# Performance work log

Measured on AMD Instinct MI355X. Metric: run time of the kernel, lower is better.

Reference implementation:

```python
import jax, jax.numpy as jnp
import numpy as np

EPS = 1e-6
NUM_HEADS = 16


def layer_norm(x, a, b):
    # Faithful to the custom LayerNorm: unbiased std (ddof=1), eps added to sigma.
    mu = jnp.mean(x, axis=-1, keepdims=True)
    sigma = jnp.std(x, axis=-1, keepdims=True, ddof=1) + EPS
    return (x - mu) / sigma * a + b


def entmax15(x):
    # Exact 1.5-entmax along the last axis (Peters et al. 2019, sort-based).
    S = x.shape[-1]
    x = x / 2.0
    x = x - jnp.max(x, axis=-1, keepdims=True)  # shift-invariant stabilization
    xs = jnp.flip(jnp.sort(x, axis=-1), axis=-1)  # descending
    k = jnp.arange(1, S + 1, dtype=x.dtype)
    mean = jnp.cumsum(xs, axis=-1) / k
    meansq = jnp.cumsum(xs * xs, axis=-1) / k
    ss = k * (meansq - mean * mean)
    delta = (1.0 - ss) / k
    tau = mean - jnp.sqrt(jnp.clip(delta, 0.0))
    support_size = jnp.sum((tau <= xs).astype(jnp.int32), axis=-1, keepdims=True)
    tau_star = jnp.take_along_axis(tau, support_size - 1, axis=-1)
    return jnp.clip(x - tau_star, 0.0) ** 2


def linear(x, w, b):
    return jnp.einsum('bsd,od->bso', x, w) + b


def setup_inputs() -> dict:
    key = jax.random.key(0)
    B, S, D, DFF = 1, 2048, 1024, 4096
    ks = jax.random.split(key, 12)
    p = lambda k, shape: jax.random.normal(k, shape, dtype=jnp.float32) * 0.02
    return {
        'inputs': jax.random.normal(ks[0], (B, S, D), dtype=jnp.float32),
        'mask': jax.random.randint(ks[1], (B, S), 0, 2, dtype=jnp.int32),
        'wq': p(ks[2], (D, D)), 'bq': jnp.zeros((D,), jnp.float32),
        'wk': p(ks[3], (D, D)), 'bk': jnp.zeros((D,), jnp.float32),
        'wv': p(ks[4], (D, D)), 'bv': jnp.zeros((D,), jnp.float32),
        'wo': p(ks[5], (D, D)), 'bo': jnp.zeros((D,), jnp.float32),
        'ln1_a': jnp.ones((D,), jnp.float32), 'ln1_b': jnp.zeros((D,), jnp.float32),
        'w1': p(ks[6], (DFF, D)), 'b1': jnp.zeros((DFF,), jnp.float32),
        'w2': p(ks[7], (D, DFF)), 'b2': jnp.zeros((D,), jnp.float32),
        'ln2_a': jnp.ones((D,), jnp.float32), 'ln2_b': jnp.zeros((D,), jnp.float32),
    }


def reference(inputs, mask, wq, bq, wk, bk, wv, bv, wo, bo, ln1_a, ln1_b,
              w1, b1, w2, b2, ln2_a, ln2_b):
    B, S, D = inputs.shape
    H = NUM_HEADS
    hd = D // H

    # --- Sublayer 1: pre-norm -> SparseMHA -> residual (dropout=0 -> identity) ---
    x1 = layer_norm(inputs, ln1_a, ln1_b)
    split = lambda t: t.reshape(B, S, H, hd).transpose(0, 2, 1, 3)  # [B,H,S,hd]
    q = split(linear(x1, wq, bq))
    k = split(linear(x1, wk, bk))
    v = split(linear(x1, wv, bv))

    scores = jnp.einsum('bhqd,bhkd->bhqk', q, k) / jnp.sqrt(jnp.asarray(hd, jnp.float32))
    # torch: mask.unsqueeze(0) -> (1,B,S); with B==1 it broadcasts as a key mask (1,1,1,S)
    mask4 = mask[None, None]  # (1,1,B,S), B==1
    scores = jnp.where(mask4 == 0, jnp.float32(-1e9), scores)

    p_attn = entmax15(scores).astype(jnp.float32)
    attended = jnp.einsum('bhqk,bhkd->bhqd', p_attn, v)
    attended = attended.transpose(0, 2, 1, 3).reshape(B, S, D)
    y = inputs + linear(attended, wo, bo)

    # --- Sublayer 2: pre-norm -> FFN -> residual ---
    x2 = layer_norm(y, ln2_a, ln2_b)
    ffn = linear(jax.nn.relu(linear(x2, w1, b1)), w2, b2)
    return y + ffn
```

## Files before the change

### kernel.cpp

```cpp
#include <hip/hip_runtime.h>
#include <hip/hip_bf16.h>

#define S   2048
#define D   1024
#define DFF 4096
#define NH  16
#define HD  64

typedef unsigned short u16;
typedef unsigned int   u32;
typedef __attribute__((ext_vector_type(8))) short      short8;
typedef __attribute__((ext_vector_type(4))) float      floatx4;
typedef __attribute__((ext_vector_type(2))) _Float16   half2v;
typedef __attribute__((ext_vector_type(4))) _Float16   half4v;
typedef __attribute__((ext_vector_type(8))) _Float16   half8v;

__device__ __forceinline__ float bu2f(u16 u) {
    union { u32 i; float f; } x; x.i = ((u32)u) << 16; return x.f;
}
__device__ __forceinline__ u16 f2bu(float f) {
    __hip_bfloat16 h = __float2bfloat16(f);
    return *(u16*)&h;
}
__device__ __forceinline__ u16 f2h(float f) {
    _Float16 h = (_Float16)f; return *(u16*)&h;
}
__device__ __forceinline__ float ldf(const float* p) { return *p; }
__device__ __forceinline__ float ldf(const u16* p)   { return bu2f(*p); }

__device__ __forceinline__ half2v pkrtz(float a, float b) {
    auto v = __builtin_amdgcn_cvt_pkrtz(a, b);
    union { decltype(v) i; half2v o; } u; u.i = v; return u.o;
}

__device__ __forceinline__ floatx4 mfma_f16(half8v a, half8v b, floatx4 c) {
    return __builtin_amdgcn_mfma_f32_16x16x32_f16(a, b, c, 0, 0, 0);
}
__device__ __forceinline__ float fdot2f(half2v a, half2v b, float c) {
#if __has_builtin(__builtin_amdgcn_fdot2)
    return __builtin_amdgcn_fdot2(a, b, c, false);
#else
    return c + (float)a[0] * (float)b[0] + (float)a[1] * (float)b[1];
#endif
}

template <int K>
__device__ __forceinline__ float ror16f(float v) {
    int s = __builtin_bit_cast(int, v);
    int r = __builtin_amdgcn_update_dpp(s, s, 0x120 | K, 0xF, 0xF, false);
    return __builtin_bit_cast(float, r);
}
__device__ __forceinline__ float rowsum16(float v) {
    v += ror16f<1>(v);
    v += ror16f<2>(v);
    v += ror16f<4>(v);
    v += ror16f<8>(v);
    return v;
}
__device__ __forceinline__ float rowmax16(float v) {
    v = fmaxf(v, ror16f<1>(v));
    v = fmaxf(v, ror16f<2>(v));
    v = fmaxf(v, ror16f<4>(v));
    v = fmaxf(v, ror16f<8>(v));
    return v;
}

__device__ __forceinline__ void async16(const void* g, void* l) {
    __builtin_amdgcn_global_load_lds(
        (const __attribute__((address_space(1))) u32*)g,
        (__attribute__((address_space(3))) u32*)l, 16, 0, 0);
}

#define WAITV(N) asm volatile("s_waitcnt vmcnt(" N ")" ::: "memory")
#define WAITL()  asm volatile("s_waitcnt lgkmcnt(0)" ::: "memory")
#define SBAR()   __builtin_amdgcn_s_barrier()
#define SCHED0() __builtin_amdgcn_sched_barrier(0)

__global__ __launch_bounds__(256)
void cvt_kernel(const float* __restrict__ in, u16* __restrict__ out, int n4)
{
    int i = blockIdx.x * 256 + threadIdx.x;
    if (i < n4) {
        float4 v = ((const float4*)in)[i];
        ushort4 s;
        s.x = f2bu(v.x); s.y = f2bu(v.y); s.z = f2bu(v.z); s.w = f2bu(v.w);
        ((ushort4*)out)[i] = s;
    }
}

__global__ __launch_bounds__(256)
void prep_kernel(const int* __restrict__ mask, int* __restrict__ newpos,
                 int* __restrict__ nkbuf,
                 const float* __restrict__ wq, const float* __restrict__ wk,
                 const float* __restrict__ wv, const float* __restrict__ wo,
                 u16* __restrict__ wqkvb, u16* __restrict__ wob)
{
    const int blk = blockIdx.x;
    const int t = threadIdx.x;
    if (blk == 0) {
        __shared__ int ps[256];
        int loc[8];
        int s = 0;
#pragma unroll
        for (int j = 0; j < 8; j++) {
            loc[j] = s;
            s += (mask[t * 8 + j] != 0);
        }
        ps[t] = s;
        __syncthreads();
        for (int off = 1; off < 256; off <<= 1) {
            int v = (t >= off) ? ps[t - off] : 0;
            __syncthreads();
            ps[t] += v;
            __syncthreads();
        }
        const int total = ps[255];
        const int base = t ? ps[t - 1] : 0;
#pragma unroll
        for (int j = 0; j < 8; j++) {
            const int gi = t * 8 + j;
            const int up = base + loc[j];
            newpos[gi] = mask[gi] ? up : (total + gi - up);
        }
        if (t == 0) nkbuf[0] = total;
    } else {
        int cb = blk - 1;
        const float* src;
        u16* dst;
        if (cb < 1024)      { src = wq; dst = wqkvb; }
        else if (cb < 2048) { src = wk; dst = wqkvb + 1024 * 1024; cb -= 1024; }
        else if (cb < 3072) { src = wv; dst = wqkvb + 2 * 1024 * 1024; cb -= 2048; }
        else                { src = wo; dst = wob; cb -= 3072; }
        const int i = cb * 256 + t;
        float4 v = ((const float4*)src)[i];
        ushort4 sv;
        sv.x = f2bu(v.x); sv.y = f2bu(v.y); sv.z = f2bu(v.z); sv.w = f2bu(v.w);
        ((ushort4*)dst)[i] = sv;
    }
}

template <typename T>
__global__ __launch_bounds__(256, 4)
void ln_kernel(const T* __restrict__ in, const float* __restrict__ ga,
               const float* __restrict__ gb, u16* __restrict__ out)
{
    const int row = blockIdx.x;
    const int t = threadIdx.x;
    const T* x = in + (size_t)row * D;
    float v[4];
    float s = 0.f, ss = 0.f;
#pragma unroll
    for (int j = 0; j < 4; j++) {
        float val = ldf(x + t + 256 * j);
        v[j] = val; s += val; ss = fmaf(val, val, ss);
    }
#pragma unroll
    for (int off = 32; off >= 1; off >>= 1) {
        s  += __shfl_down(s,  off, 64);
        ss += __shfl_down(ss, off, 64);
    }
    __shared__ float red[10];
    const int wave = t >> 6, lane = t & 63;
    if (lane == 0) { red[wave] = s; red[4 + wave] = ss; }
    __syncthreads();
    if (t == 0) {
        float S1 = red[0] + red[1] + red[2] + red[3];
        float S2 = red[4] + red[5] + red[6] + red[7];
        float mu = S1 / (float)D;
        float var = (S2 - (float)D * mu * mu) / (float)(D - 1);
        float sig = sqrtf(fmaxf(var, 0.f)) + 1e-6f;
        red[8] = mu; red[9] = 1.f / sig;
    }
    __syncthreads();
    const float mu = red[8], rs = red[9];
#pragma unroll
    for (int j = 0; j < 4; j++) {
        int c = t + 256 * j;
        out[(size_t)row * D + c] = f2bu((v[j] - mu) * rs * ga[c] + gb[c]);
    }
}

#define GEMM_CORE(A_, B_, K_)                                                   \
    __shared__ u16 As[3 * 128 * 32];                                            \
    __shared__ u16 Bs[3 * 128 * 32];                                            \
    const int t = threadIdx.x;                                                  \
    const int w = t >> 6, l = t & 63;                                           \
    const int m0 = blockIdx.y * 128, n0 = blockIdx.x * 128;                     \
    const int qk = l >> 4, col = l & 15;                                        \
    const int wm = (w & 1) * 64, wn = (w >> 1) * 64;                            \
    const int sr  = l >> 2;                                                     \
    const int sq  = l & 3;                                                      \
    const int row = w * 16 + sr;                                                \
    const int gq  = sq ^ ((row >> 1) & 3);                                      \
    const u16* Ap = A_ + (size_t)(m0 + row) * K_ + gq * 8;                      \
    const u16* Bp = B_ + (size_t)(n0 + row) * K_ + gq * 8;                      \
    u16* AsW = As + w * 16 * 32;                                                \
    u16* BsW = Bs + w * 16 * 32;                                                \
    const int mloc = wm + col, nloc = wn + col;                                 \
    const int aoff = mloc * 32 + (qk ^ ((mloc >> 1) & 3)) * 8;                  \
    const int boff = nloc * 32 + (qk ^ ((nloc >> 1) & 3)) * 8;                  \
    floatx4 acc[4][4];                                                          \
    _Pragma("unroll")                                                           \
    for (int i = 0; i < 4; i++)                                                 \
        _Pragma("unroll")                                                       \
        for (int j = 0; j < 4; j++) acc[i][j] = (floatx4)0.f;                   \
    const int NT_ = K_ / 32;                                                    \
    _Pragma("unroll")                                                           \
    for (int s = 0; s < 3; s++) {                                               \
        async16(Ap,                   AsW + s * 4096);                          \
        async16(Ap + (size_t)64 * K_, AsW + s * 4096 + 64 * 32);                \
        async16(Bp,                   BsW + s * 4096);                          \
        async16(Bp + (size_t)64 * K_, BsW + s * 4096 + 64 * 32);                \
        Ap += 32; Bp += 32;                                                     \
    }                                                                           \
    WAITV("8"); SCHED0(); SBAR();                                               \
    int cur = 0;                                                                \
    for (int t0 = 0; t0 + 3 < NT_; ++t0) {                                      \
        short8 a[4], b[4];                                                      \
        const u16* aB = As + cur * 4096 + aoff;                                 \
        const u16* bB = Bs + cur * 4096 + boff;                                 \
        _Pragma("unroll")                                                       \
        for (int i = 0; i < 4; i++) a[i] = *(const short8*)(aB + i * 16 * 32);  \
        _Pragma("unroll")                                                       \
        for (int j = 0; j < 4; j++) b[j] = *(const short8*)(bB + j * 16 * 32);  \
        WAITL(); SCHED0(); SBAR();                                              \
        async16(Ap,                   AsW + cur * 4096);                        \
        async16(Ap + (size_t)64 * K_, AsW + cur * 4096 + 64 * 32);              \
        async16(Bp,                   BsW + cur * 4096);                        \
        async16(Bp + (size_t)64 * K_, BsW + cur * 4096 + 64 * 32);              \
        Ap += 32; Bp += 32;                                                     \
        _Pragma("unroll")                                                       \
        for (int i = 0; i < 4; i++)                                             \
            _Pragma("unroll")                                                   \
            for (int j = 0; j < 4; j++)                                         \
                acc[i][j] = __builtin_amdgcn_mfma_f32_16x16x32_bf16(            \
                    a[i], b[j], acc[i][j], 0, 0, 0);                            \
        WAITV("8"); SCHED0(); SBAR();                                           \
        cur = cur + 1; if (cur == 3) cur = 0;                                   \
    }                                                                           \
    _Pragma("unroll")                                                           \
    for (int tail = 0; tail < 3; tail++) {                                      \
        short8 a[4], b[4];                                                      \
        const u16* aB = As + cur * 4096 + aoff;                                 \
        const u16* bB = Bs + cur * 4096 + boff;                                 \
        _Pragma("unroll")                                                       \
        for (int i = 0; i < 4; i++) a[i] = *(const short8*)(aB + i * 16 * 32);  \
        _Pragma("unroll")                                                       \
        for (int j = 0; j < 4; j++) b[j] = *(const short8*)(bB + j * 16 * 32);  \
        _Pragma("unroll")                                                       \
        for (int i = 0; i < 4; i++)                                             \
            _Pragma("unroll")                                                   \
            for (int j = 0; j < 4; j++)                                         \
                acc[i][j] = __builtin_amdgcn_mfma_f32_16x16x32_bf16(            \
                    a[i], b[j], acc[i][j], 0, 0, 0);                            \
        if (tail == 0) { WAITV("4"); SCHED0(); SBAR(); }                        \
        if (tail == 1) { WAITV("0"); SCHED0(); SBAR(); }                        \
        cur = cur + 1; if (cur == 3) cur = 0;                                   \
    }

template <int OMODE, bool RELU, int RES>
__global__ __launch_bounds__(256, 2)
void gemm_mfma(const u16* __restrict__ A, const u16* __restrict__ B,
               const float* __restrict__ bias, const void* __restrict__ res,
               void* __restrict__ Cout, int M, int N, int K)
{
    GEMM_CORE(A, B, K)
#pragma unroll
    for (int j = 0; j < 4; j++) {
        const int n = n0 + wn + j * 16 + col;
        const float bn = bias[n];
#pragma unroll
        for (int i = 0; i < 4; i++) {
#pragma unroll
            for (int r = 0; r < 4; r++) {
                const int m = m0 + wm + i * 16 + qk * 4 + r;
                float v = acc[i][j][r] + bn;
                if (RELU) v = fmaxf(v, 0.f);
                if (RES == 1) v += ((const float*)res)[(size_t)m * N + n];
                if (RES == 2) v += bu2f(((const u16*)res)[(size_t)m * N + n]);
                if (OMODE == 0) ((float*)Cout)[(size_t)m * N + n] = v;
                if (OMODE == 1) ((u16*)Cout)[(size_t)m * N + n] = f2bu(v);
            }
        }
    }
}

__global__ __launch_bounds__(256, 2)
void gemm_qkv(const u16* __restrict__ A, const u16* __restrict__ B,
              const float* __restrict__ bq, const float* __restrict__ bk,
              const float* __restrict__ bv, const int* __restrict__ np,
              u16* __restrict__ outQ, u16* __restrict__ outK,
              u16* __restrict__ outVT)
{
    const int K = D;
    GEMM_CORE(A, B, K)
    const int seg   = n0 >> 10;
    const int nbase = n0 & 1023;
    const float* bs = (seg == 0) ? bq : (seg == 1) ? bk : bv;
    int npm[4][4];
    if (seg != 0) {
#pragma unroll
        for (int i = 0; i < 4; i++)
#pragma unroll
            for (int r = 0; r < 4; r++)
                npm[i][r] = np[m0 + wm + i * 16 + qk * 4 + r];
    }
#pragma unroll
    for (int j = 0; j < 4; j++) {
        const int nl = nbase + wn + j * 16 + col;
        const float bn = bs[nl];
#pragma unroll
        for (int i = 0; i < 4; i++) {
#pragma unroll
            for (int r = 0; r < 4; r++) {
                const int m = m0 + wm + i * 16 + qk * 4 + r;
                float v = acc[i][j][r] + bn;
                if (seg == 0)      outQ [(size_t)m * D + nl]          = f2h(v);
                else if (seg == 1) outK [(size_t)npm[i][r] * D + nl]  = f2h(v);
                else               outVT[(size_t)nl * S + npm[i][r]]  = f2h(v);
            }
        }
    }
}

template <int OMODE, int RES>
__global__ __launch_bounds__(256, 2)
void gemm_mfma64(const u16* __restrict__ A, const u16* __restrict__ B,
                 const float* __restrict__ bias, const void* __restrict__ res,
                 void* __restrict__ Cout, int M, int N, int K)
{
    __shared__ u16 As[3 * 128 * 32];
    __shared__ u16 Bs[3 * 64 * 32];
    const int t = threadIdx.x;
    const int w = t >> 6, l = t & 63;
    const int m0 = blockIdx.y * 128, n0 = blockIdx.x * 64;
    const int qk = l >> 4, col = l & 15;
    const int wm = (w & 1) * 64, wn = (w >> 1) * 32;
    const int sr = l >> 2, sq = l & 3;
    const int row = w * 16 + sr;
    const int gq = sq ^ ((row >> 1) & 3);
    const u16* Ap = A + (size_t)(m0 + row) * K + gq * 8;
    const u16* Bp = B + (size_t)(n0 + row) * K + gq * 8;
    u16* AsW = As + w * 16 * 32;
    u16* BsW = Bs + w * 16 * 32;
    const int mloc = wm + col, nloc = wn + col;
    const int aoff = mloc * 32 + (qk ^ ((mloc >> 1) & 3)) * 8;
    const int boff = nloc * 32 + (qk ^ ((nloc >> 1) & 3)) * 8;
    floatx4 acc[4][2];
#pragma unroll
    for (int i = 0; i < 4; i++)
#pragma unroll
        for (int j = 0; j < 2; j++) acc[i][j] = (floatx4)0.f;
    const int NT_ = K / 32;
#pragma unroll
    for (int s = 0; s < 3; s++) {
        async16(Ap,                  AsW + s * 4096);
        async16(Ap + (size_t)64 * K, AsW + s * 4096 + 64 * 32);
        async16(Bp,                  BsW + s * 2048);
        Ap += 32; Bp += 32;
    }
    WAITV("6"); SCHED0(); SBAR();
    int cur = 0;
    for (int t0 = 0; t0 + 3 < NT_; ++t0) {
        short8 a[4], b[2];
        const u16* aB = As + cur * 4096 + aoff;
        const u16* bB = Bs + cur * 2048 + boff;
#pragma unroll
        for (int i = 0; i < 4; i++) a[i] = *(const short8*)(aB + i * 16 * 32);
#pragma unroll
        for (int j = 0; j < 2; j++) b[j] = *(const short8*)(bB + j * 16 * 32);
        WAITL(); SCHED0(); SBAR();
        async16(Ap,                  AsW + cur * 4096);
        async16(Ap + (size_t)64 * K, AsW + cur * 4096 + 64 * 32);
        async16(Bp,                  BsW + cur * 2048);
        Ap += 32; Bp += 32;
#pragma unroll
        for (int i = 0; i < 4; i++)
#pragma unroll
            for (int j = 0; j < 2; j++)
                acc[i][j] = __builtin_amdgcn_mfma_f32_16x16x32_bf16(
                    a[i], b[j], acc[i][j], 0, 0, 0);
        WAITV("6"); SCHED0(); SBAR();
        cur = cur + 1; if (cur == 3) cur = 0;
    }
#pragma unroll
    for (int tail = 0; tail < 3; tail++) {
        short8 a[4], b[2];
        const u16* aB = As + cur * 4096 + aoff;
        const u16* bB = Bs + cur * 2048 + boff;
#pragma unroll
        for (int i = 0; i < 4; i++) a[i] = *(const short8*)(aB + i * 16 * 32);
#pragma unroll
        for (int j = 0; j < 2; j++) b[j] = *(const short8*)(bB + j * 16 * 32);
#pragma unroll
        for (int i = 0; i < 4; i++)
#pragma unroll
            for (int j = 0; j < 2; j++)
                acc[i][j] = __builtin_amdgcn_mfma_f32_16x16x32_bf16(
                    a[i], b[j], acc[i][j], 0, 0, 0);
        if (tail == 0) { WAITV("3"); SCHED0(); SBAR(); }
        if (tail == 1) { WAITV("0"); SCHED0(); SBAR(); }
        cur = cur + 1; if (cur == 3) cur = 0;
    }
#pragma unroll
    for (int j = 0; j < 2; j++) {
        const int n = n0 + wn + j * 16 + col;
        const float bn = bias[n];
#pragma unroll
        for (int i = 0; i < 4; i++) {
#pragma unroll
            for (int r = 0; r < 4; r++) {
                const int m = m0 + wm + i * 16 + qk * 4 + r;
                float v = acc[i][j][r] + bn;
                if (RES == 1) v += ((const float*)res)[(size_t)m * N + n];
                if (RES == 2) v += bu2f(((const u16*)res)[(size_t)m * N + n]);
                if (OMODE == 0) ((float*)Cout)[(size_t)m * N + n] = v;
                if (OMODE == 1) ((u16*)Cout)[(size_t)m * N + n] = f2bu(v);
            }
        }
    }
}

__global__ __launch_bounds__(256, 3)
void attn_cvt(const u16* __restrict__ qb, const u16* __restrict__ kb,
              const u16* __restrict__ vT, const int* __restrict__ nkbuf,
              u16* __restrict__ att,
              const float* __restrict__ w1src, u16* __restrict__ w1dst)
{
    __shared__ u16 Plds[16 * 1024];
    const int blk = blockIdx.x;
    const int t  = threadIdx.x;
    if (blk >= 2048) {
        const int i = (blk - 2048) * 256 + t;
        float4 v = ((const float4*)w1src)[i];
        ushort4 sv;
        sv.x = f2bu(v.x); sv.y = f2bu(v.y); sv.z = f2bu(v.z); sv.w = f2bu(v.w);
        ((ushort4*)w1dst)[i] = sv;
        return;
    }
    const int nk = nkbuf[0];
    const int NS = (nk + 127) >> 7;
    const int NT = (nk + 31) >> 5;
    const int hh = blk >> 7;
    const int q0 = (blk & 127) * 16;
    const int w  = __builtin_amdgcn_readfirstlane(t >> 6);
    const int l  = t & 63;
    const int lg = l >> 4, lc = l & 15;
    const _Float16 NEG = (_Float16)(-30000.f);
    const half4v NEG4 = {NEG, NEG, NEG, NEG};

    const u16* qp = qb + (size_t)(q0 + lc) * D + hh * HD + lg * 8;
    const half8v bq0 = *(const half8v*)qp;
    const half8v bq1 = *(const half8v*)(qp + 32);
    const u16* kbase = kb + hh * HD + lg * 8;
    const int R = 4 * w + lg;
    const half2v one2 = {(_Float16)1.f, (_Float16)1.f};
    const u16* vp = vT + (size_t)(hh * HD + w * 16 + lc) * S + lg * 8;

    if (nk <= 1152) {
#pragma unroll
        for (int T = 0; T < 16; T++) {
            const int g = 4 * T + w;
            if (g < 8 * NS) {
                half4v scv;
                if ((g + 1) * 16 <= nk) {
                    const u16* kp = kbase + (size_t)(g * 16 + lc) * D;
                    floatx4 a = (floatx4)0.f;
                    a = mfma_f16(*(const half8v*)kp,        bq0, a);
                    a = mfma_f16(*(const half8v*)(kp + 32), bq1, a);
                    half2v p01 = pkrtz(a[0] * 0.0625f, a[1] * 0.0625f);
                    half2v p23 = pkrtz(a[2] * 0.0625f, a[3] * 0.0625f);
                    scv = __builtin_shufflevector(p01, p23, 0, 1, 2, 3);
                } else if (g * 16 < nk) {
                    const u16* kp = kbase + (size_t)(g * 16 + lc) * D;
                    floatx4 a = (floatx4)0.f;
                    a = mfma_f16(*(const half8v*)kp,        bq0, a);
                    a = mfma_f16(*(const half8v*)(kp + 32), bq1, a);
                    const int kb0 = g * 16 + lg * 4;
                    half2v p01 = pkrtz(kb0 + 0 < nk ? a[0] * 0.0625f : -30000.f,
                                       kb0 + 1 < nk ? a[1] * 0.0625f : -30000.f);
                    half2v p23 = pkrtz(kb0 + 2 < nk ? a[2] * 0.0625f : -30000.f,
                                       kb0 + 3 < nk ? a[3] * 0.0625f : -30000.f);
                    scv = __builtin_shufflevector(p01, p23, 0, 1, 2, 3);
                } else {
                    scv = NEG4;
                }
                const int kl = g * 16 + lg * 4;
                const int b  = kl >> 3;
                const int p  = b ^ ((b >> 3) & 7) ^ (lc & 7);
                *(half4v*)&Plds[lc * 1024 + p * 8 + (lg & 1) * 4] = scv;
            }
        }
        __syncthreads();

        half8v xq[9];
#pragma unroll
        for (int s = 0; s < 8; s++) {
            if (s < NS) {
                const int b = 16 * s + lc;
                const int p = b ^ ((b >> 3) & 7) ^ (R & 7);
                xq[s] = *(const half8v*)&Plds[R * 1024 + p * 8];
            }
        }
        if (NS > 8) {
            __syncthreads();
#pragma unroll
            for (int T = 16; T < 18; T++) {
                const int g = 4 * T + w;
                half4v scv;
                if ((g + 1) * 16 <= nk) {
                    const u16* kp = kbase + (size_t)(g * 16 + lc) * D;
                    floatx4 a = (floatx4)0.f;
                    a = mfma_f16(*(const half8v*)kp,        bq0, a);
                    a = mfma_f16(*(const half8v*)(kp + 32), bq1, a);
                    half2v p01 = pkrtz(a[0] * 0.0625f, a[1] * 0.0625f);
                    half2v p23 = pkrtz(a[2] * 0.0625f, a[3] * 0.0625f);
                    scv = __builtin_shufflevector(p01, p23, 0, 1, 2, 3);
                } else if (g * 16 < nk) {
                    const u16* kp = kbase + (size_t)(g * 16 + lc) * D;
                    floatx4 a = (floatx4)0.f;
                    a = mfma_f16(*(const half8v*)kp,        bq0, a);
                    a = mfma_f16(*(const half8v*)(kp + 32), bq1, a);
                    const int kb0 = g * 16 + lg * 4;
                    half2v p01 = pkrtz(kb0 + 0 < nk ? a[0] * 0.0625f : -30000.f,
                                       kb0 + 1 < nk ? a[1] * 0.0625f : -30000.f);
                    half2v p23 = pkrtz(kb0 + 2 < nk ? a[2] * 0.0625f : -30000.f,
                                       kb0 + 3 < nk ? a[3] * 0.0625f : -30000.f);
                    scv = __builtin_shufflevector(p01, p23, 0, 1, 2, 3);
                } else {
                    scv = NEG4;
                }
                const int kl = g * 16 + lg * 4 - 1024;
                const int b  = kl >> 3;
                const int p  = b ^ ((b >> 3) & 7) ^ (lc & 7);
                *(half4v*)&Plds[lc * 1024 + p * 8 + (lg & 1) * 4] = scv;
            }
            __syncthreads();
            {
                const int b = lc;
                const int p = b ^ ((b >> 3) & 7) ^ (R & 7);
                xq[8] = *(const half8v*)&Plds[R * 1024 + p * 8];
            }
        }

        float tau;
        {
            half8v m8 = xq[0];
#pragma unroll
            for (int i = 1; i < 9; i++)
                if (i < NS) m8 = __builtin_elementwise_max(m8, xq[i]);
            union { half8v v; half2v h[4]; } u; u.v = m8;
            half2v m2 = __builtin_elementwise_max(
                __builtin_elementwise_max(u.h[0], u.h[1]),
                __builtin_elementwise_max(u.h[2], u.h[3]));
            float mx = fmaxf((float)m2[0], (float)m2[1]);
            mx = rowmax16(mx);
            tau = mx - 1.0f;
        }

        const float nact = (float)(8 * NS);
#pragma unroll 1
        for (int it = 0; it < 12; it++) {
            const _Float16 th = (_Float16)tau;
            const float tf = (float)th;
            const half8v t8 = {th, th, th, th, th, th, th, th};
            float m1a = 0.f, m1b = 0.f, m2a = 0.f, m2b = 0.f;
#pragma unroll
            for (int i = 0; i < 9; i++) {
                if (i < NS) {
                    union { half8v v; half2v h[4]; } u;
                    u.v = __builtin_elementwise_max(xq[i], t8);
                    m1a = fdot2f(u.h[0], one2, m1a);
                    m2a = fdot2f(u.h[0], u.h[0], m2a);
                    m1b = fdot2f(u.h[1], one2, m1b);
                    m2b = fdot2f(u.h[1], u.h[1], m2b);
                    m1a = fdot2f(u.h[2], one2, m1a);
                    m2a = fdot2f(u.h[2], u.h[2], m2a);
                    m1b = fdot2f(u.h[3], one2, m1b);
                    m2b = fdot2f(u.h[3], u.h[3], m2b);
                }
            }
            const float M1 = m1a + m1b, M2 = m2a + m2b;
            float s1 = fmaf(-nact, tf, M1);
            float s2 = fmaf(tf, fmaf(nact, tf, -2.f * M1), M2);
            s1 = rowsum16(s1);
            s2 = rowsum16(s2);
            const float delta = (s2 - 1.0f) / (2.0f * fmaxf(s1, 1e-4f));
            tau += delta;
            if (__all(fabsf(delta) < 2.5e-4f)) break;
        }

        const _Float16 th = (_Float16)tau;
        const half8v t8 = {th, th, th, th, th, th, th, th};
        const half8v z8 = (half8v)(_Float16)0.f;
        floatx4 oa0 = (floatx4)0.f, oa1 = (floatx4)0.f;
        floatx4 oa2 = (floatx4)0.f, oa3 = (floatx4)0.f;
#pragma unroll
        for (int s = 0; s < 8; s++) {
            if (s < NS) {
                half8v dp = __builtin_elementwise_max(xq[s] - t8, z8);
                const int b = 16 * s + lc;
                const int p = b ^ ((b >> 3) & 7) ^ (R & 7);
                *(half8v*)&Plds[R * 1024 + p * 8] = dp * dp;
            }
        }
        __syncthreads();
        __builtin_amdgcn_s_setprio(1);
#pragma unroll
        for (int kt = 0; kt < 32; kt++) {
            if (kt < NT) {
                const int b = kt * 4 + lg;
                const int p = b ^ ((b >> 3) & 7) ^ (lc & 7);
                half8v af = *(const half8v*)&Plds[lc * 1024 + p * 8];
                half8v bf = *(const half8v*)(vp + kt * 32);
                if ((kt & 3) == 0)      oa0 = mfma_f16(af, bf, oa0);
                else if ((kt & 3) == 1) oa1 = mfma_f16(af, bf, oa1);
                else if ((kt & 3) == 2) oa2 = mfma_f16(af, bf, oa2);
                else                    oa3 = mfma_f16(af, bf, oa3);
            }
        }
        __builtin_amdgcn_s_setprio(0);
        if (NS > 8) {
            __syncthreads();
            {
                half8v dp = __builtin_elementwise_max(xq[8] - t8, z8);
                const int b = lc;
                const int p = b ^ ((b >> 3) & 7) ^ (R & 7);
                *(half8v*)&Plds[R * 1024 + p * 8] = dp * dp;
            }
            __syncthreads();
            const u16* vph = vp + 1024;
#pragma unroll
            for (int kt2 = 0; kt2 < 4; kt2++) {
                if (32 + kt2 < NT) {
                    const int b = kt2 * 4 + lg;
                    const int p = b ^ ((b >> 3) & 7) ^ (lc & 7);
                    half8v af = *(const half8v*)&Plds[lc * 1024 + p * 8];
                    half8v bf = *(const half8v*)(vph + kt2 * 32);
                    if ((kt2 & 3) == 0)      oa0 = mfma_f16(af, bf, oa0);
                    else if ((kt2 & 3) == 1) oa1 = mfma_f16(af, bf, oa1);
                    else if ((kt2 & 3) == 2) oa2 = mfma_f16(af, bf, oa2);
                    else                     oa3 = mfma_f16(af, bf, oa3);
                }
            }
        }
        const floatx4 oacc = (oa0 + oa1) + (oa2 + oa3);
#pragma unroll
        for (int r = 0; r < 4; r++)
            att[(size_t)(q0 + lg * 4 + r) * D + hh * HD + w * 16 + lc] =
                f2bu(oacc[r]);
    } else {
        half4v sc[32];
        {
            __builtin_amdgcn_s_setprio(1);
#pragma unroll
            for (int T = 0; T < 32; T++) {
                const int g = 4 * T + w;
                if (g * 16 < nk) {
                    const u16* kp = kbase + (size_t)(g * 16 + lc) * D;
                    floatx4 a = (floatx4)0.f;
                    a = mfma_f16(*(const half8v*)kp,        bq0, a);
                    a = mfma_f16(*(const half8v*)(kp + 32), bq1, a);
                    const int kb0 = g * 16 + lg * 4;
                    half2v p01 = pkrtz(kb0 + 0 < nk ? a[0] * 0.0625f : -30000.f,
                                       kb0 + 1 < nk ? a[1] * 0.0625f : -30000.f);
                    half2v p23 = pkrtz(kb0 + 2 < nk ? a[2] * 0.0625f : -30000.f,
                                       kb0 + 3 < nk ? a[3] * 0.0625f : -30000.f);
                    sc[T] = __builtin_shufflevector(p01, p23, 0, 1, 2, 3);
                } else {
                    sc[T] = NEG4;
                }
            }
            __builtin_amdgcn_s_setprio(0);
        }

        half8v xq[16];
        {
#pragma unroll
            for (int T = 0; T < 16; T++) {
                const int g  = 4 * T + w;
                const int kl = g * 16 + lg * 4;
                const int b  = kl >> 3;
                const int p  = b ^ ((b >> 3) & 7) ^ (lc & 7);
                *(half4v*)&Plds[lc * 1024 + p * 8 + (lg & 1) * 4] = sc[T];
            }
            __syncthreads();
#pragma unroll
            for (int s = 0; s < 8; s++) {
                if (s < NS) {
                    const int b = 16 * s + lc;
                    const int p = b ^ ((b >> 3) & 7) ^ (R & 7);
                    xq[s] = *(const half8v*)&Plds[R * 1024 + p * 8];
                }
            }
            __syncthreads();
#pragma unroll
            for (int T = 16; T < 32; T++) {
                const int g  = 4 * T + w;
                const int kl = g * 16 + lg * 4 - 1024;
                const int b  = kl >> 3;
                const int p  = b ^ ((b >> 3) & 7) ^ (lc & 7);
                *(half4v*)&Plds[lc * 1024 + p * 8 + (lg & 1) * 4] = sc[T];
            }
            __syncthreads();
#pragma unroll
            for (int s = 0; s < 8; s++) {
                const int j = 8 + s;
                if (j < NS) {
                    const int b = 16 * s + lc;
                    const int p = b ^ ((b >> 3) & 7) ^ (R & 7);
                    xq[j] = *(const half8v*)&Plds[R * 1024 + p * 8];
                }
            }
        }

        float tau;
        {
            half8v m8 = xq[0];
#pragma unroll
            for (int i = 1; i < 16; i++)
                if (i < NS) m8 = __builtin_elementwise_max(m8, xq[i]);
            union { half8v v; half2v h[4]; } u; u.v = m8;
            half2v m2 = __builtin_elementwise_max(
                __builtin_elementwise_max(u.h[0], u.h[1]),
                __builtin_elementwise_max(u.h[2], u.h[3]));
            float mx = fmaxf((float)m2[0], (float)m2[1]);
            mx = rowmax16(mx);
            tau = mx - 1.0f;
        }

        const float nact = (float)(8 * NS);
#pragma unroll 1
        for (int it = 0; it < 12; it++) {
            const _Float16 th = (_Float16)tau;
            const float tf = (float)th;
            const half8v t8 = {th, th, th, th, th, th, th, th};
            float m1a = 0.f, m1b = 0.f, m2a = 0.f, m2b = 0.f;
#pragma unroll
            for (int i = 0; i < 16; i++) {
                if (i < NS) {
                    union { half8v v; half2v h[4]; } u;
                    u.v = __builtin_elementwise_max(xq[i], t8);
                    m1a = fdot2f(u.h[0], one2, m1a);
                    m2a = fdot2f(u.h[0], u.h[0], m2a);
                    m1b = fdot2f(u.h[1], one2, m1b);
                    m2b = fdot2f(u.h[1], u.h[1], m2b);
                    m1a = fdot2f(u.h[2], one2, m1a);
                    m2a = fdot2f(u.h[2], u.h[2], m2a);
                    m1b = fdot2f(u.h[3], one2, m1b);
                    m2b = fdot2f(u.h[3], u.h[3], m2b);
                }
            }
            const float M1 = m1a + m1b, M2 = m2a + m2b;
            float s1 = fmaf(-nact, tf, M1);
            float s2 = fmaf(tf, fmaf(nact, tf, -2.f * M1), M2);
            s1 = rowsum16(s1);
            s2 = rowsum16(s2);
            const float delta = (s2 - 1.0f) / (2.0f * fmaxf(s1, 1e-4f));
            tau += delta;
            if (__all(fabsf(delta) < 2.5e-4f)) break;
        }

        const _Float16 th = (_Float16)tau;
        const half8v t8 = {th, th, th, th, th, th, th, th};
        const half8v z8 = (half8v)(_Float16)0.f;
        floatx4 oa0 = (floatx4)0.f, oa1 = (floatx4)0.f;
        floatx4 oa2 = (floatx4)0.f, oa3 = (floatx4)0.f;
#pragma unroll
        for (int s = 0; s < 8; s++) {
            if (s < NS) {
                half8v dp = __builtin_elementwise_max(xq[s] - t8, z8);
                const int b = 16 * s + lc;
                const int p = b ^ ((b >> 3) & 7) ^ (R & 7);
                *(half8v*)&Plds[R * 1024 + p * 8] = dp * dp;
            }
        }
        __syncthreads();
        __builtin_amdgcn_s_setprio(1);
#pragma unroll
        for (int kt = 0; kt < 32; kt++) {
            if (kt < NT) {
                const int b = kt * 4 + lg;
                const int p = b ^ ((b >> 3) & 7) ^ (lc & 7);
                half8v af = *(const half8v*)&Plds[lc * 1024 + p * 8];
                half8v bf = *(const half8v*)(vp + kt * 32);
                if ((kt & 3) == 0)      oa0 = mfma_f16(af, bf, oa0);
                else if ((kt & 3) == 1) oa1 = mfma_f16(af, bf, oa1);
                else if ((kt & 3) == 2) oa2 = mfma_f16(af, bf, oa2);
                else                    oa3 = mfma_f16(af, bf, oa3);
            }
        }
        __builtin_amdgcn_s_setprio(0);
        {
            __syncthreads();
#pragma unroll
            for (int s = 0; s < 8; s++) {
                const int j = 8 + s;
                if (j < NS) {
                    half8v dp = __builtin_elementwise_max(xq[j] - t8, z8);
                    const int b = 16 * s + lc;
                    const int p = b ^ ((b >> 3) & 7) ^ (R & 7);
                    *(half8v*)&Plds[R * 1024 + p * 8] = dp * dp;
                }
            }
            __syncthreads();
            const u16* vph = vp + 1024;
            __builtin_amdgcn_s_setprio(1);
#pragma unroll
            for (int kt = 0; kt < 32; kt++) {
                if (32 + kt < NT) {
                    const int b = kt * 4 + lg;
                    const int p = b ^ ((b >> 3) & 7) ^ (lc & 7);
                    half8v af = *(const half8v*)&Plds[lc * 1024 + p * 8];
                    half8v bf = *(const half8v*)(vph + kt * 32);
                    if ((kt & 3) == 0)      oa0 = mfma_f16(af, bf, oa0);
                    else if ((kt & 3) == 1) oa1 = mfma_f16(af, bf, oa1);
                    else if ((kt & 3) == 2) oa2 = mfma_f16(af, bf, oa2);
                    else                    oa3 = mfma_f16(af, bf, oa3);
                }
            }
            __builtin_amdgcn_s_setprio(0);
        }
        const floatx4 oacc = (oa0 + oa1) + (oa2 + oa3);
#pragma unroll
        for (int r = 0; r < 4; r++)
            att[(size_t)(q0 + lg * 4 + r) * D + hh * HD + w * 16 + lc] =
                f2bu(oacc[r]);
    }
}

extern "C" void kernel_launch(void* const* d_in, const int* in_sizes, int n_in,
                              void* d_out, int out_size, void* d_ws, size_t ws_size,
                              hipStream_t stream)
{
    const float* inp  = (const float*)d_in[0];
    const int*   mask = (const int*)d_in[1];
    const float* wq   = (const float*)d_in[2];
    const float* bq   = (const float*)d_in[3];
    const float* wk   = (const float*)d_in[4];
    const float* bk   = (const float*)d_in[5];
    const float* wv   = (const float*)d_in[6];
    const float* bv   = (const float*)d_in[7];
    const float* wo   = (const float*)d_in[8];
    const float* bo   = (const float*)d_in[9];
    const float* ln1a = (const float*)d_in[10];
    const float* ln1b = (const float*)d_in[11];
    const float* w1   = (const float*)d_in[12];
    const float* b1   = (const float*)d_in[13];
    const float* w2   = (const float*)d_in[14];
    const float* b2   = (const float*)d_in[15];
    const float* ln2a = (const float*)d_in[16];
    const float* ln2b = (const float*)d_in[17];

    const size_t MB = 1u << 20;
    char* w = (char*)d_ws;
    u16* wqkvb = (u16*)(w + 0 * MB);
    u16* w1b   = (u16*)(w + 0 * MB);
    u16* w2b   = (u16*)(w + 0 * MB);
    u16* x1    = (u16*)(w + 8 * MB);
    u16* att   = x1;
    u16* x2    = x1;
    u16* qb_   = (u16*)(w + 12 * MB);
    u16* yb    = (u16*)(w + 12 * MB);
    u16* kb_   = (u16*)(w + 16 * MB);
    u16* vTb   = (u16*)(w + 20 * MB);
    u16* wob   = (u16*)(w + 24 * MB);
    u16* hb    = (u16*)(w + 16 * MB);
    int* np    = (int*)(w + 26 * MB);
    int* nkbuf = np + 2048;
    float* outF = (float*)d_out;

    prep_kernel<<<4097, 256, 0, stream>>>(mask, np, nkbuf, wq, wk, wv, wo,
                                          wqkvb, wob);
    ln_kernel<float><<<S, 256, 0, stream>>>(inp, ln1a, ln1b, x1);
    gemm_qkv<<<dim3(3 * D / 128, S / 128), 256, 0, stream>>>(
        x1, wqkvb, bq, bk, bv, np, qb_, kb_, vTb);
    attn_cvt<<<2048 + 4096, 256, 0, stream>>>(qb_, kb_, vTb, nkbuf, att,
                                              w1, w1b);
    gemm_mfma64<1, 1><<<dim3(D / 64, S / 128), 256, 0, stream>>>(
        att, wob, bo, inp, yb, S, D, D);
    ln_kernel<u16><<<S, 256, 0, stream>>>(yb, ln2a, ln2b, x2);
    gemm_mfma<1, true, 0><<<dim3(DFF / 128, S / 128), 256, 0, stream>>>(
        x2, w1b, b1, nullptr, hb, S, DFF, D);
    cvt_kernel<<<4096, 256, 0, stream>>>(w2, w2b, (DFF * D) / 4);
    gemm_mfma64<0, 2><<<dim3(D / 64, S / 128), 256, 0, stream>>>(
        hb, w2b, b2, yb, outF, S, D, DFF);
}
```

Before: 324.1 us.

## Fuse LN1 and W2 conversion into prep kernel; shrink output GEMM tiles

Folds the first LayerNorm and, when the workspace is large enough, the W2 fp32-to-bf16 conversion into the prep kernel, which removes two kernel launches and lets these independent jobs run side by side. The two 64-wide-N GEMMs (output projection and FFN down-projection) switch from 128x64 to 64x64 tiles with 4-block occupancy, so the grid has 512 blocks instead of 256 and more CUs are busy. In exchange, smaller tiles reuse less data per load, and the W2 copy needs extra workspace starting at 32MB.

Result: faster. 314.9 us (-2.8%).

```diff
diff --git a/kernel.cpp b/kernel.cpp
--- a/kernel.cpp
+++ b/kernel.cpp
@@ -93,7 +93,10 @@
                  int* __restrict__ nkbuf,
                  const float* __restrict__ wq, const float* __restrict__ wk,
                  const float* __restrict__ wv, const float* __restrict__ wo,
-                 u16* __restrict__ wqkvb, u16* __restrict__ wob)
+                 u16* __restrict__ wqkvb, u16* __restrict__ wob,
+                 const float* __restrict__ inp, const float* __restrict__ ln1a,
+                 const float* __restrict__ ln1b, u16* __restrict__ x1,
+                 const float* __restrict__ w2, u16* __restrict__ w2dst)
 {
     const int blk = blockIdx.x;
     const int t = threadIdx.x;
@@ -123,7 +126,7 @@
             newpos[gi] = mask[gi] ? up : (total + gi - up);
         }
         if (t == 0) nkbuf[0] = total;
-    } else {
+    } else if (blk <= 4096) {
         int cb = blk - 1;
         const float* src;
         u16* dst;
@@ -136,6 +139,46 @@
         ushort4 sv;
         sv.x = f2bu(v.x); sv.y = f2bu(v.y); sv.z = f2bu(v.z); sv.w = f2bu(v.w);
         ((ushort4*)dst)[i] = sv;
+    } else if (blk <= 6144) {
+        const int rrow = blk - 4097;
+        const float* x = inp + (size_t)rrow * D;
+        float v[4];
+        float s = 0.f, ss = 0.f;
+#pragma unroll
+        for (int j = 0; j < 4; j++) {
+            float val = x[t + 256 * j];
+            v[j] = val; s += val; ss = fmaf(val, val, ss);
+        }
+#pragma unroll
+        for (int off = 32; off >= 1; off >>= 1) {
+            s  += __shfl_down(s,  off, 64);
+            ss += __shfl_down(ss, off, 64);
+        }
+        __shared__ float red[10];
+        const int wave = t >> 6, lane = t & 63;
+        if (lane == 0) { red[wave] = s; red[4 + wave] = ss; }
+        __syncthreads();
+        if (t == 0) {
+            float S1 = red[0] + red[1] + red[2] + red[3];
+            float S2 = red[4] + red[5] + red[6] + red[7];
+            float mu = S1 / (float)D;
+            float var = (S2 - (float)D * mu * mu) / (float)(D - 1);
+            float sig = sqrtf(fmaxf(var, 0.f)) + 1e-6f;
+            red[8] = mu; red[9] = 1.f / sig;
+        }
+        __syncthreads();
+        const float mu = red[8], rs = red[9];
+#pragma unroll
+        for (int j = 0; j < 4; j++) {
+            int c = t + 256 * j;
+            x1[(size_t)rrow * D + c] = f2bu((v[j] - mu) * rs * ln1a[c] + ln1b[c]);
+        }
+    } else {
+        const int i = (blk - 6145) * 256 + t;
+        float4 v = ((const float4*)w2)[i];
+        ushort4 sv;
+        sv.x = f2bu(v.x); sv.y = f2bu(v.y); sv.z = f2bu(v.z); sv.w = f2bu(v.w);
+        ((ushort4*)w2dst)[i] = sv;
     }
 }
 
@@ -324,18 +367,18 @@
 }
 
 template <int OMODE, int RES>
-__global__ __launch_bounds__(256, 2)
-void gemm_mfma64(const u16* __restrict__ A, const u16* __restrict__ B,
-                 const float* __restrict__ bias, const void* __restrict__ res,
-                 void* __restrict__ Cout, int M, int N, int K)
+__global__ __launch_bounds__(256, 4)
+void gemm64(const u16* __restrict__ A, const u16* __restrict__ B,
+            const float* __restrict__ bias, const void* __restrict__ res,
+            void* __restrict__ Cout, int M, int N, int K)
 {
-    __shared__ u16 As[3 * 128 * 32];
+    __shared__ u16 As[3 * 64 * 32];
     __shared__ u16 Bs[3 * 64 * 32];
     const int t = threadIdx.x;
     const int w = t >> 6, l = t & 63;
-    const int m0 = blockIdx.y * 128, n0 = blockIdx.x * 64;
+    const int m0 = blockIdx.y * 64, n0 = blockIdx.x * 64;
     const int qk = l >> 4, col = l & 15;
-    const int wm = (w & 1) * 64, wn = (w >> 1) * 32;
+    const int wm = (w & 1) * 32, wn = (w >> 1) * 32;
     const int sr = l >> 2, sq = l & 3;
     const int row = w * 16 + sr;
     const int gq = sq ^ ((row >> 1) & 3);
@@ -346,59 +389,57 @@
     const int mloc = wm + col, nloc = wn + col;
     const int aoff = mloc * 32 + (qk ^ ((mloc >> 1) & 3)) * 8;
     const int boff = nloc * 32 + (qk ^ ((nloc >> 1) & 3)) * 8;
-    floatx4 acc[4][2];
-#pragma unroll
-    for (int i = 0; i < 4; i++)
+    floatx4 acc[2][2];
+#pragma unroll
+    for (int i = 0; i < 2; i++)
 #pragma unroll
         for (int j = 0; j < 2; j++) acc[i][j] = (floatx4)0.f;
     const int NT_ = K / 32;
 #pragma unroll
     for (int s = 0; s < 3; s++) {
-        async16(Ap,                  AsW + s * 4096);
-        async16(Ap + (size_t)64 * K, AsW + s * 4096 + 64 * 32);
-        async16(Bp,                  BsW + s * 2048);
+        async16(Ap, AsW + s * 2048);
+        async16(Bp, BsW + s * 2048);
         Ap += 32; Bp += 32;
     }
-    WAITV("6"); SCHED0(); SBAR();
+    WAITV("4"); SCHED0(); SBAR();
     int cur = 0;
     for (int t0 = 0; t0 + 3 < NT_; ++t0) {
-        short8 a[4], b[2];
-        const u16* aB = As + cur * 4096 + aoff;
+        short8 a[2], b[2];
+        const u16* aB = As + cur * 2048 + aoff;
         const u16* bB = Bs + cur * 2048 + boff;
 #pragma unroll
-        for (int i = 0; i < 4; i++) a[i] = *(const short8*)(aB + i * 16 * 32);
+        for (int i = 0; i < 2; i++) a[i] = *(const short8*)(aB + i * 16 * 32);
 #pragma unroll
         for (int j = 0; j < 2; j++) b[j] = *(const short8*)(bB + j * 16 * 32);
         WAITL(); SCHED0(); SBAR();
-        async16(Ap,                  AsW + cur * 4096);
-        async16(Ap + (size_t)64 * K, AsW + cur * 4096 + 64 * 32);
-        async16(Bp,                  BsW + cur * 2048);
+        async16(Ap, AsW + cur * 2048);
+        async16(Bp, BsW + cur * 2048);
         Ap += 32; Bp += 32;
 #pragma unroll
-        for (int i = 0; i < 4; i++)
+        for (int i = 0; i < 2; i++)
 #pragma unroll
             for (int j = 0; j < 2; j++)
                 acc[i][j] = __builtin_amdgcn_mfma_f32_16x16x32_bf16(
                     a[i], b[j], acc[i][j], 0, 0, 0);
-        WAITV("6"); SCHED0(); SBAR();
+        WAITV("4"); SCHED0(); SBAR();
         cur = cur + 1; if (cur == 3) cur = 0;
     }
 #pragma unroll
     for (int tail = 0; tail < 3; tail++) {
-        short8 a[4], b[2];
-        const u16* aB = As + cur * 4096 + aoff;
+        short8 a[2], b[2];
+        const u16* aB = As + cur * 2048 + aoff;
         const u16* bB = Bs + cur * 2048 + boff;
 #pragma unroll
-        for (int i = 0; i < 4; i++) a[i] = *(const short8*)(aB + i * 16 * 32);
+        for (int i = 0; i < 2; i++) a[i] = *(const short8*)(aB + i * 16 * 32);
 #pragma unroll
         for (int j = 0; j < 2; j++) b[j] = *(const short8*)(bB + j * 16 * 32);
 #pragma unroll
-        for (int i = 0; i < 4; i++)
+        for (int i = 0; i < 2; i++)
 #pragma unroll
             for (int j = 0; j < 2; j++)
                 acc[i][j] = __builtin_amdgcn_mfma_f32_16x16x32_bf16(
                     a[i], b[j], acc[i][j], 0, 0, 0);
-        if (tail == 0) { WAITV("3"); SCHED0(); SBAR(); }
+        if (tail == 0) { WAITV("2"); SCHED0(); SBAR(); }
         if (tail == 1) { WAITV("0"); SCHED0(); SBAR(); }
         cur = cur + 1; if (cur == 3) cur = 0;
     }
@@ -407,7 +448,7 @@
         const int n = n0 + wn + j * 16 + col;
         const float bn = bias[n];
 #pragma unroll
-        for (int i = 0; i < 4; i++) {
+        for (int i = 0; i < 2; i++) {
 #pragma unroll
             for (int r = 0; r < 4; r++) {
                 const int m = m0 + wm + i * 16 + qk * 4 + r;
@@ -856,7 +897,6 @@
     char* w = (char*)d_ws;
     u16* wqkvb = (u16*)(w + 0 * MB);
     u16* w1b   = (u16*)(w + 0 * MB);
-    u16* w2b   = (u16*)(w + 0 * MB);
     u16* x1    = (u16*)(w + 8 * MB);
     u16* att   = x1;
     u16* x2    = x1;
@@ -870,19 +910,23 @@
     int* nkbuf = np + 2048;
     float* outF = (float*)d_out;
 
-    prep_kernel<<<4097, 256, 0, stream>>>(mask, np, nkbuf, wq, wk, wv, wo,
-                                          wqkvb, wob);
-    ln_kernel<float><<<S, 256, 0, stream>>>(inp, ln1a, ln1b, x1);
+    const bool w2early = (ws_size >= 40 * MB);
+    u16* w2b = w2early ? (u16*)(w + 32 * MB) : (u16*)(w + 0 * MB);
+
+    prep_kernel<<<w2early ? 10241 : 6145, 256, 0, stream>>>(
+        mask, np, nkbuf, wq, wk, wv, wo, wqkvb, wob,
+        inp, ln1a, ln1b, x1, w2, w2b);
     gemm_qkv<<<dim3(3 * D / 128, S / 128), 256, 0, stream>>>(
         x1, wqkvb, bq, bk, bv, np, qb_, kb_, vTb);
     attn_cvt<<<2048 + 4096, 256, 0, stream>>>(qb_, kb_, vTb, nkbuf, att,
                                               w1, w1b);
-    gemm_mfma64<1, 1><<<dim3(D / 64, S / 128), 256, 0, stream>>>(
+    gemm64<1, 1><<<dim3(D / 64, S / 64), 256, 0, stream>>>(
         att, wob, bo, inp, yb, S, D, D);
     ln_kernel<u16><<<S, 256, 0, stream>>>(yb, ln2a, ln2b, x2);
     gemm_mfma<1, true, 0><<<dim3(DFF / 128, S / 128), 256, 0, stream>>>(
         x2, w1b, b1, nullptr, hb, S, DFF, D);
-    cvt_kernel<<<4096, 256, 0, stream>>>(w2, w2b, (DFF * D) / 4);
-    gemm_mfma64<0, 2><<<dim3(D / 64, S / 128), 256, 0, stream>>>(
+    if (!w2early)
+        cvt_kernel<<<4096, 256, 0, stream>>>(w2, w2b, (DFF * D) / 4);
+    gemm64<0, 2><<<dim3(D / 64, S / 64), 256, 0, stream>>>(
         hb, w2b, b2, yb, outF, S, D, DFF);
 }
```
